# Optimization experiments

Measured on AMD Instinct MI355X. Metric: run time of the kernel, lower is better.

Reference implementation:

```python
import jax, jax.numpy as jnp
import numpy as np

ALPHA = 2.0   # spikingjelly surrogate.ATan default alpha
TAU = 2.0
VTH = 1.0
EPS = 1e-5

@jax.custom_vjp
def atan_spike(x):
    return (x >= 0.0).astype(x.dtype)

def _as_fwd(x):
    return atan_spike(x), x

def _as_bwd(x, g):
    # ATan surrogate derivative: alpha/2 / (1 + (pi/2*alpha*x)^2)
    return (g * (ALPHA / 2.0) / (1.0 + (jnp.pi / 2.0 * ALPHA * x) ** 2),)

atan_spike.defvjp(_as_fwd, _as_bwd)

def lif_multistep(x):
    # x: [B, T, D]; LIF with decay_input=True, v_reset=0 (hard reset), detach_reset=True
    xt = jnp.swapaxes(x, 0, 1)  # [T, B, D] time-major
    def step(v, xi):
        v = v + (xi - v) / TAU                       # integrate with input decay
        s = atan_spike(v - VTH)                       # fire (surrogate grad)
        v = v * (1.0 - jax.lax.stop_gradient(s))      # hard reset to 0, detached
        return v, s
    _, spikes = jax.lax.scan(step, jnp.zeros_like(xt[0]), xt)
    return jnp.swapaxes(spikes, 0, 1)  # [B, T, D]

def layernorm(x, g, b):
    m = x.mean(-1, keepdims=True)
    v = x.var(-1, keepdims=True)
    return (x - m) / jnp.sqrt(v + EPS) * g + b

def setup_inputs() -> dict:
    key = jax.random.key(0)
    ks = jax.random.split(key, 6)
    B, T, IN, HP, E, H, D = 256, 256, 4, 64, 512, 1024, 4
    s = 0.02
    return {
        "hist_feat": jax.random.normal(ks[0], (B, T, IN), jnp.float32),
        "pW1": jax.random.normal(ks[1], (IN, HP), jnp.float32) * s,
        "pb1": jnp.zeros((HP,), jnp.float32),
        "pW2": jax.random.normal(ks[2], (HP, E), jnp.float32) * s,
        "pb2": jnp.zeros((E,), jnp.float32),
        "fc1_w": jax.random.normal(ks[3], (D, E, H), jnp.float32) * s,
        "fc1_b": jnp.zeros((D, H), jnp.float32),
        "ln1_g": jnp.ones((D, H), jnp.float32),
        "ln1_b": jnp.zeros((D, H), jnp.float32),
        "fc2_w": jax.random.normal(ks[4], (D, H, E), jnp.float32) * s,
        "fc2_b": jnp.zeros((D, E), jnp.float32),
        "ln2_g": jnp.ones((D, E), jnp.float32),
        "ln2_b": jnp.zeros((D, E), jnp.float32),
    }

def reference(hist_feat, pW1, pb1, pW2, pb2, fc1_w, fc1_b, ln1_g, ln1_b,
              fc2_w, fc2_b, ln2_g, ln2_b):
    # input projector: Linear -> exact GELU -> Linear
    x = jax.nn.gelu(hist_feat @ pW1 + pb1, approximate=False) @ pW2 + pb2  # [B,T,E]
    depth = fc1_w.shape[0]
    for d in range(depth):  # small fixed layer loop
        res = x
        h = layernorm(x @ fc1_w[d] + fc1_b[d], ln1_g[d], ln1_b[d])  # [B,T,H]
        h = lif_multistep(h)
        h = layernorm(h @ fc2_w[d] + fc2_b[d], ln2_g[d], ln2_b[d])  # [B,T,E]
        h = lif_multistep(h)
        x = res + h  # dropout is identity in eval mode
    return x[:, -1]  # pooling='last', no mask -> last timestep, [B,E]
```

## Files before the change

kernel.cpp:

```cpp
#include <hip/hip_runtime.h>
#include <hip/hip_bf16.h>
#include <math.h>

#define B_  256
#define T_  256
#define IN_ 4
#define HP_ 64
#define E_  512
#define H_  1024
#define D_  4

typedef __hip_bfloat16 bf16;
typedef _Float16 f16;
typedef _Float16 f16x8 __attribute__((ext_vector_type(8)));
typedef float f32x4 __attribute__((ext_vector_type(4)));

__device__ __forceinline__ float load1(const void* p, size_t idx, bool isb) {
    if (isb) {
        unsigned int u = ((const unsigned short*)p)[idx];
        return __uint_as_float(u << 16);
    }
    return ((const float*)p)[idx];
}

__device__ __forceinline__ float4 load4(const void* p, size_t idx, bool isb) {
    if (isb) {
        ushort4 u = *(const ushort4*)((const unsigned short*)p + idx);
        float4 r;
        r.x = __uint_as_float(((unsigned int)u.x) << 16);
        r.y = __uint_as_float(((unsigned int)u.y) << 16);
        r.z = __uint_as_float(((unsigned int)u.z) << 16);
        r.w = __uint_as_float(((unsigned int)u.w) << 16);
        return r;
    }
    return *((const float4*)p + (idx >> 2));
}

__device__ __forceinline__ void split3(float x, f16& h, f16& hs, f16& lb) {
    h = (f16)x;
    float hf = (float)h;
    hs = (f16)(hf * 4.8828125e-4f);
    lb = (f16)((x - hf) * 2048.0f);
}

__global__ void sniff_count_kernel(const unsigned short* __restrict__ p,
                                   int* __restrict__ cnts) {
    __shared__ int cnt;
    if (threadIdx.x == 0) cnt = 0;
    __syncthreads();
    int local = 0;
    #pragma unroll
    for (int k = 0; k < 4; ++k) {
        int i = blockIdx.x * 1024 + k * 256 + threadIdx.x;
        unsigned int bits = ((unsigned int)p[i]) << 16;
        float v = __uint_as_float(bits);
        float a = fabsf(v);
        if (!(a <= 1e4f)) local++;
        else if (v != 0.0f && a < 1e-6f) local++;
    }
    atomicAdd(&cnt, local);
    __syncthreads();
    if (threadIdx.x == 0) cnts[blockIdx.x] = cnt;
}

__global__ void sniff_final_kernel(const int* __restrict__ cnts,
                                   int* __restrict__ flag) {
    int s = 0;
    for (int i = 0; i < 64; ++i) s += cnts[i];
    *flag = (s > 1024) ? 0 : 1;
}

__global__ __launch_bounds__(256) void wsplit_kernel(
        const void* __restrict__ W, size_t wOff, unsigned short* __restrict__ Wt,
        int K, int N, const int* __restrict__ flag) {
    const bool isb = (*flag != 0);
    __shared__ float tile[32][33];
    const int n0 = blockIdx.x * 32, k0 = blockIdx.y * 32;
    const int t = threadIdx.x;
    {
        int lk = t >> 3, ln0 = (t & 7) << 2;
        float4 v = load4(W, wOff + (size_t)(k0 + lk) * N + n0 + ln0, isb);
        tile[lk][ln0 + 0] = v.x; tile[lk][ln0 + 1] = v.y;
        tile[lk][ln0 + 2] = v.z; tile[lk][ln0 + 3] = v.w;
    }
    __syncthreads();
    int n = t >> 3, kq0 = (t & 7) << 2;
    size_t base = (size_t)(n0 + n) * (2 * (size_t)K) + k0 + kq0;
    #pragma unroll
    for (int j = 0; j < 4; ++j) {
        float x = tile[kq0 + j][n];
        f16 h, hs, lb;
        split3(x, h, hs, lb);
        Wt[base + j]     = *(unsigned short*)&h;
        Wt[base + j + K] = *(unsigned short*)&lb;
    }
}

__global__ __launch_bounds__(512, 2) void gemm_mfma3_kernel(
        const unsigned short* __restrict__ At, const unsigned short* __restrict__ Wt,
        const void* __restrict__ bias, size_t bOff,
        float* __restrict__ C, int N, int K, const int* __restrict__ flag) {
    const bool isb = (*flag != 0);
    __shared__ unsigned short As[128 * 64];
    __shared__ unsigned short Bs[128 * 64];

    const int gx = N >> 7;
    const int gy = (int)gridDim.x / gx;
    int bx, by;
    {
        int bid = blockIdx.x;
        if ((gy & 7) == 0) {
            int k = bid & 7, i = bid >> 3;
            bx = i % gx;
            by = (gy >> 3) * k + i / gx;
        } else { bx = bid % gx; by = bid / gx; }
    }
    const int bn = bx * 128;
    const int bm = by * 128;

    const int tid  = threadIdx.x;
    const int lane = tid & 63;
    const int wave = tid >> 6;
    const int wm = wave >> 1;
    const int wn = wave & 1;
    const int g  = lane >> 4;
    const int lr = lane & 15;

    const int sar = tid >> 2;
    const int skq = tid & 3;

    const f16 C11 = (f16)4.8828125e-4f;
    const f16x8 c11v = {C11, C11, C11, C11, C11, C11, C11, C11};

    f32x4 acc[2][4];
    #pragma unroll
    for (int i = 0; i < 2; ++i)
        #pragma unroll
        for (int j = 0; j < 4; ++j) acc[i][j] = (f32x4){0.f, 0.f, 0.f, 0.f};

    const unsigned short* Ap = At + (size_t)(bm + sar) * (2 * (size_t)K) + skq * 8;
    const unsigned short* Wp = Wt + (size_t)(bn + sar) * (2 * (size_t)K) + skq * 8;

    f16x8 av0 = *(const f16x8*)(Ap);
    f16x8 av1 = *(const f16x8*)(Ap + K);
    f16x8 wv0 = *(const f16x8*)(Wp);
    f16x8 wv1 = *(const f16x8*)(Wp + K);

    const int nt = K >> 5;
    for (int t = 0; t < nt; ++t) {
        const int arb = sar * 64, asw = sar & 7;
        *(f16x8*)&As[arb + ((skq ^ asw)) * 8]       = av0;
        *(f16x8*)&As[arb + (((4 | skq) ^ asw)) * 8] = av1;
        *(f16x8*)&Bs[arb + ((skq ^ asw)) * 8]       = wv0;
        *(f16x8*)&Bs[arb + (((4 | skq) ^ asw)) * 8] = wv1;
        __syncthreads();
        if (t + 1 < nt) {
            const int k0 = (t + 1) << 5;
            av0 = *(const f16x8*)(Ap + k0);
            av1 = *(const f16x8*)(Ap + K + k0);
            wv0 = *(const f16x8*)(Wp + k0);
            wv1 = *(const f16x8*)(Wp + K + k0);
        }
        f16x8 a0[2], a2[2], b0[4], b2[4];
        #pragma unroll
        for (int mi = 0; mi < 2; ++mi) {
            const int ar = wm * 32 + mi * 16 + lr;
            a0[mi] = *(const f16x8*)&As[ar * 64 + ((g ^ (ar & 7))) * 8];
            a2[mi] = *(const f16x8*)&As[ar * 64 + (((4 | g) ^ (ar & 7))) * 8];
        }
        #pragma unroll
        for (int ni = 0; ni < 4; ++ni) {
            const int br = wn * 64 + ni * 16 + lr;
            b0[ni] = *(const f16x8*)&Bs[br * 64 + ((g ^ (br & 7))) * 8];
            b2[ni] = *(const f16x8*)&Bs[br * 64 + (((4 | g) ^ (br & 7))) * 8];
        }
        #pragma unroll
        for (int mi = 0; mi < 2; ++mi)
            #pragma unroll
            for (int ni = 0; ni < 4; ++ni)
                acc[mi][ni] = __builtin_amdgcn_mfma_f32_16x16x32_f16(
                    a0[mi], b0[ni], acc[mi][ni], 0, 0, 0);
        {
            f16x8 a1[2];
            #pragma unroll
            for (int mi = 0; mi < 2; ++mi) a1[mi] = a0[mi] * c11v;
            #pragma unroll
            for (int mi = 0; mi < 2; ++mi)
                #pragma unroll
                for (int ni = 0; ni < 4; ++ni)
                    acc[mi][ni] = __builtin_amdgcn_mfma_f32_16x16x32_f16(
                        a1[mi], b2[ni], acc[mi][ni], 0, 0, 0);
        }
        {
            f16x8 b1[4];
            #pragma unroll
            for (int ni = 0; ni < 4; ++ni) b1[ni] = b0[ni] * c11v;
            #pragma unroll
            for (int mi = 0; mi < 2; ++mi)
                #pragma unroll
                for (int ni = 0; ni < 4; ++ni)
                    acc[mi][ni] = __builtin_amdgcn_mfma_f32_16x16x32_f16(
                        a2[mi], b1[ni], acc[mi][ni], 0, 0, 0);
        }
        __syncthreads();
    }
    #pragma unroll
    for (int ni = 0; ni < 4; ++ni) {
        const int col = bn + wn * 64 + ni * 16 + lr;
        const float bv = load1(bias, bOff + col, isb);
        #pragma unroll
        for (int mi = 0; mi < 2; ++mi) {
            #pragma unroll
            for (int r = 0; r < 4; ++r) {
                const size_t row = (size_t)(bm + wm * 32 + mi * 16 + g * 4 + r);
                C[row * N + col] = acc[mi][ni][r] + bv;
            }
        }
    }
}

__global__ __launch_bounds__(256, 3) void gemm_mfma2_kernel(
        const unsigned short* __restrict__ At, const unsigned short* __restrict__ Wt,
        const void* __restrict__ bias, size_t bOff,
        float* __restrict__ C, int N, int K, const int* __restrict__ flag) {
    const bool isb = (*flag != 0);
    __shared__ unsigned short As[2][128 * 64];
    __shared__ unsigned short Bs[2][128 * 64];

    const int gx = N >> 7;
    const int gy = (int)gridDim.x / gx;
    int bx, by;
    {
        int bid = blockIdx.x;
        if ((gy & 7) == 0) {
            int k = bid & 7, i = bid >> 3;
            bx = i % gx;
            by = (gy >> 3) * k + i / gx;
        } else { bx = bid % gx; by = bid / gx; }
    }
    const int bn = bx * 128;
    const int bm = by * 128;

    const int tid  = threadIdx.x;
    const int lane = tid & 63;
    const int wave = tid >> 6;
    const int wm = wave >> 1;
    const int wn = wave & 1;
    const int g  = lane >> 4;
    const int lr = lane & 15;

    const int sar = tid >> 1;
    const int sah = tid & 1;
    const int sbn = tid >> 1;
    const int sq  = tid & 1;

    const f16 C11 = (f16)4.8828125e-4f;
    const f16x8 c11v = {C11, C11, C11, C11, C11, C11, C11, C11};

    f32x4 acc[4][4];
    #pragma unroll
    for (int i = 0; i < 4; ++i)
        #pragma unroll
        for (int j = 0; j < 4; ++j) acc[i][j] = (f32x4){0.f, 0.f, 0.f, 0.f};

    const unsigned short* Ap = At + (size_t)(bm + sar) * (size_t)K + sah * 16;
    const unsigned short* Wp = Wt + (size_t)(bn + sbn) * (2 * (size_t)K) + sq * 16;

    f16x8 av[2], wv[4];
    #pragma unroll
    for (int c = 0; c < 2; ++c)
        av[c] = *(const f16x8*)(Ap + c * 8);
    #pragma unroll
    for (int pl = 0; pl < 2; ++pl)
        #pragma unroll
        for (int c = 0; c < 2; ++c)
            wv[pl * 2 + c] = *(const f16x8*)(Wp + (size_t)pl * K + c * 8);

    const int nt = K >> 5;
    for (int t = 0; t < nt; ++t) {
        const int cur = t & 1;
        const int arb = sar * 64, asw = sar & 7;
        #pragma unroll
        for (int c = 0; c < 2; ++c) {
            const int gg = sah * 2 + c;
            *(f16x8*)&As[cur][arb + ((gg ^ asw)) * 8] = av[c];
        }
        const int brb = sbn * 64, bsw = sbn & 7;
        #pragma unroll
        for (int pl = 0; pl < 2; ++pl)
            #pragma unroll
            for (int c = 0; c < 2; ++c) {
                const int gg = sq * 2 + c;
                *(f16x8*)&Bs[cur][brb + (((pl << 2) | gg) ^ bsw) * 8] = wv[pl * 2 + c];
            }
        __syncthreads();
        if (t + 1 < nt) {
            const int k0 = (t + 1) << 5;
            #pragma unroll
            for (int c = 0; c < 2; ++c)
                av[c] = *(const f16x8*)(Ap + k0 + c * 8);
            #pragma unroll
            for (int pl = 0; pl < 2; ++pl)
                #pragma unroll
                for (int c = 0; c < 2; ++c)
                    wv[pl * 2 + c] = *(const f16x8*)(Wp + (size_t)pl * K + k0 + c * 8);
        }
        f16x8 a0[4], b0[4], b2[4];
        #pragma unroll
        for (int mi = 0; mi < 4; ++mi) {
            const int ar = wm * 64 + mi * 16 + lr;
            a0[mi] = *(const f16x8*)&As[cur][ar * 64 + ((g ^ (ar & 7))) * 8];
        }
        #pragma unroll
        for (int ni = 0; ni < 4; ++ni) {
            const int br = wn * 64 + ni * 16 + lr;
            b0[ni] = *(const f16x8*)&Bs[cur][br * 64 + ((g ^ (br & 7))) * 8];
            b2[ni] = *(const f16x8*)&Bs[cur][br * 64 + (((4 | g) ^ (br & 7))) * 8];
        }
        #pragma unroll
        for (int mi = 0; mi < 4; ++mi)
            #pragma unroll
            for (int ni = 0; ni < 4; ++ni)
                acc[mi][ni] = __builtin_amdgcn_mfma_f32_16x16x32_f16(
                    a0[mi], b0[ni], acc[mi][ni], 0, 0, 0);
        {
            f16x8 a1[4];
            #pragma unroll
            for (int mi = 0; mi < 4; ++mi) a1[mi] = a0[mi] * c11v;
            #pragma unroll
            for (int mi = 0; mi < 4; ++mi)
                #pragma unroll
                for (int ni = 0; ni < 4; ++ni)
                    acc[mi][ni] = __builtin_amdgcn_mfma_f32_16x16x32_f16(
                        a1[mi], b2[ni], acc[mi][ni], 0, 0, 0);
        }
    }
    #pragma unroll
    for (int ni = 0; ni < 4; ++ni) {
        const int col = bn + wn * 64 + ni * 16 + lr;
        const float bv = load1(bias, bOff + col, isb);
        #pragma unroll
        for (int mi = 0; mi < 4; ++mi) {
            #pragma unroll
            for (int r = 0; r < 4; ++r) {
                const size_t row = (size_t)(bm + wm * 64 + mi * 16 + g * 4 + r);
                C[row * N + col] = acc[mi][ni][r] + bv;
            }
        }
    }
}

#define RB_ 16
__global__ __launch_bounds__(256) void proj_kernel(
        const void* __restrict__ hist, const void* __restrict__ pW1,
        const void* __restrict__ pb1,  const void* __restrict__ pW2,
        const void* __restrict__ pb2,  float* __restrict__ Xc,
        unsigned short* __restrict__ At1,
        size_t m0, const int* __restrict__ flag) {
    const bool isb = (*flag != 0);
    __shared__ float h1[RB_][HP_];
    const size_t mb = (size_t)blockIdx.x * RB_;
    const int tid = threadIdx.x;
    const int lane = tid & 63;
    const int grp = tid >> 6;
    #pragma unroll
    for (int rep = 0; rep < 4; ++rep) {
        int idx = tid + rep * 256;
        int r = idx >> 6, c = idx & 63;
        size_t gm = m0 + mb + r;
        float acc = 0.f;
        #pragma unroll
        for (int i = 0; i < IN_; ++i)
            acc = fmaf(load1(hist, gm * IN_ + i, isb),
                       load1(pW1, (size_t)i * HP_ + c, isb), acc);
        acc += load1(pb1, c, isb);
        h1[r][c] = 0.5f * acc * (1.0f + erff(acc * 0.70710678118654752440f));
    }
    __syncthreads();
    const int e0 = lane * 8;
    float acc[4][8];
    #pragma unroll
    for (int r = 0; r < 4; ++r)
        #pragma unroll
        for (int j = 0; j < 8; ++j) acc[r][j] = 0.f;
    for (int i = 0; i < HP_; ++i) {
        float4 wA = load4(pW2, (size_t)i * E_ + e0, isb);
        float4 wB = load4(pW2, (size_t)i * E_ + e0 + 4, isb);
        float w[8] = {wA.x, wA.y, wA.z, wA.w, wB.x, wB.y, wB.z, wB.w};
        #pragma unroll
        for (int r = 0; r < 4; ++r) {
            float h = h1[grp * 4 + r][i];
            #pragma unroll
            for (int j = 0; j < 8; ++j) acc[r][j] = fmaf(h, w[j], acc[r][j]);
        }
    }
    #pragma unroll
    for (int r = 0; r < 4; ++r) {
        size_t row = mb + grp * 4 + r;
        float o[8];
        #pragma unroll
        for (int j = 0; j < 8; ++j)
            o[j] = acc[r][j] + load1(pb2, e0 + j, isb);
        *(float4*)(Xc + row * E_ + e0)     = (float4){o[0], o[1], o[2], o[3]};
        *(float4*)(Xc + row * E_ + e0 + 4) = (float4){o[4], o[5], o[6], o[7]};
        f16x8 hv, lv;
        #pragma unroll
        for (int j = 0; j < 8; ++j) {
            f16 h, hs, lb;
            split3(o[j], h, hs, lb);
            hv[j] = h; lv[j] = lb;
        }
        *(f16x8*)&At1[row * (2 * E_) + e0]      = hv;
        *(f16x8*)&At1[row * (2 * E_) + E_ + e0] = lv;
    }
}

__device__ __forceinline__ float block_sum(float v, float* smem, int tid) {
    #pragma unroll
    for (int off = 32; off > 0; off >>= 1) v += __shfl_down(v, off, 64);
    __syncthreads();
    if ((tid & 63) == 0) smem[tid >> 6] = v;
    __syncthreads();
    if (tid == 0) smem[4] = smem[0] + smem[1] + smem[2] + smem[3];
    __syncthreads();
    return smem[4];
}

__global__ __launch_bounds__(256) void ln_stats_kernel(const float* __restrict__ Y,
                                                       float* __restrict__ stats,
                                                       int N) {
    __shared__ float smem[5];
    size_t row = blockIdx.x;
    const float* y = Y + row * (size_t)N;
    int tid = threadIdx.x;
    int nPer = N >> 8;
    float vals[4];
    float s = 0.f;
    for (int i = 0; i < nPer; ++i) { float v = y[tid + (i << 8)]; vals[i] = v; s += v; }
    float mean = block_sum(s, smem, tid) / (float)N;
    float sq = 0.f;
    for (int i = 0; i < nPer; ++i) { float d0 = vals[i] - mean; sq += d0 * d0; }
    float var = block_sum(sq, smem, tid) / (float)N;
    if (tid == 0) {
        stats[row * 2]     = mean;
        stats[row * 2 + 1] = sqrtf(var + 1e-5f);
    }
}

__global__ __launch_bounds__(64) void lif_kernel(const float* __restrict__ Y,
                                                 const float* __restrict__ stats,
                                                 const void* __restrict__ g, size_t gOff,
                                                 const void* __restrict__ b, size_t bOff,
                                                 unsigned short* __restrict__ At2,
                                                 int N, const int* __restrict__ flag) {
    const bool isb = (*flag != 0);
    int f = blockIdx.x * 64 + threadIdx.x;
    int bb = blockIdx.y;
    const float gw = load1(g, gOff + f, isb);
    const float bw = load1(b, bOff + f, isb);
    size_t base = (size_t)bb * T_ * N + f;
    size_t srow = (size_t)bb * T_;
    float v = 0.f;
    for (int t0 = 0; t0 < T_; t0 += 16) {
        float x[16], mn[16], dn[16], s[16];
        #pragma unroll
        for (int j = 0; j < 16; ++j) {
            x[j]  = Y[base + (size_t)(t0 + j) * N];
            mn[j] = stats[(srow + t0 + j) * 2];
            dn[j] = stats[(srow + t0 + j) * 2 + 1];
        }
        #pragma unroll
        for (int j = 0; j < 16; ++j) {
            float xn = (x[j] - mn[j]) / dn[j] * gw + bw;
            v = v + (xn - v) * 0.5f;
            s[j] = (v - 1.0f >= 0.0f) ? 1.0f : 0.0f;
            v = v * (1.0f - s[j]);
        }
        #pragma unroll
        for (int j = 0; j < 16; ++j) {
            f16 h = (f16)s[j];
            At2[base + (size_t)(t0 + j) * N] = *(unsigned short*)&h;
        }
    }
}

__global__ __launch_bounds__(64) void lif_add_kernel(const float* __restrict__ Z,
                                                     const float* __restrict__ stats,
                                                     const void* __restrict__ g, size_t gOff,
                                                     const void* __restrict__ b, size_t bOff,
                                                     float* __restrict__ Xc,
                                                     unsigned short* __restrict__ At1,
                                                     void* __restrict__ outp, int b0,
                                                     int lastLayer,
                                                     const int* __restrict__ flag) {
    const bool isb = (*flag != 0);
    int e = blockIdx.x * 64 + threadIdx.x;
    int bb = blockIdx.y;
    const float gw = load1(g, gOff + e, isb);
    const float bw = load1(b, bOff + e, isb);
    size_t base  = (size_t)bb * T_ * E_ + e;
    size_t base2 = (size_t)bb * T_ * (2 * E_) + e;
    size_t srow  = (size_t)bb * T_;
    float v = 0.f;
    for (int t0 = 0; t0 < T_; t0 += 16) {
        float x[16], xc[16], mn[16], dn[16], s[16];
        #pragma unroll
        for (int j = 0; j < 16; ++j) {
            x[j]  = Z[base + (size_t)(t0 + j) * E_];
            mn[j] = stats[(srow + t0 + j) * 2];
            dn[j] = stats[(srow + t0 + j) * 2 + 1];
        }
        #pragma unroll
        for (int j = 0; j < 16; ++j) xc[j] = Xc[base + (size_t)(t0 + j) * E_];
        #pragma unroll
        for (int j = 0; j < 16; ++j) {
            float xn = (x[j] - mn[j]) / dn[j] * gw + bw;
            v = v + (xn - v) * 0.5f;
            s[j] = (v - 1.0f >= 0.0f) ? 1.0f : 0.0f;
            v = v * (1.0f - s[j]);
        }
        #pragma unroll
        for (int j = 0; j < 16; ++j) {
            float nx = xc[j] + s[j];
            Xc[base + (size_t)(t0 + j) * E_] = nx;
            f16 h, hs, lb;
            split3(nx, h, hs, lb);
            At1[base2 + (size_t)(t0 + j) * (2 * E_)]      = *(unsigned short*)&h;
            At1[base2 + (size_t)(t0 + j) * (2 * E_) + E_] = *(unsigned short*)&lb;
        }
        if (lastLayer && t0 + 16 == T_) {
            float nx = Xc[base + (size_t)(T_ - 1) * E_];
            size_t oi = (size_t)(b0 + bb) * E_ + e;
            if (isb) ((bf16*)outp)[oi] = __float2bfloat16(nx);
            else     ((float*)outp)[oi] = nx;
        }
    }
}

extern "C" void kernel_launch(void* const* d_in, const int* in_sizes, int n_in,
                              void* d_out, int out_size, void* d_ws, size_t ws_size,
                              hipStream_t stream) {
    char* ws = (char*)d_ws;
    int* flag = (int*)ws;
    int* cnts = (int*)(ws + 64);

    const size_t wtCount = 2 * (size_t)E_ * H_;
    const size_t wtBytes = 2 * D_ * wtCount * sizeof(unsigned short);
    unsigned short* Wt1 = (unsigned short*)(ws + 512);
    unsigned short* Wt2 = Wt1 + (size_t)D_ * wtCount;

    size_t used = 512 + wtBytes;
    size_t avail = (ws_size > used) ? ws_size - used : 0;
    const size_t perBatch = (size_t)T_ * ((E_ + H_ + E_) * 4 + 2 * E_ * 2 + H_ * 2 + 16);
    int CB = 256;
    while (CB > 1 && (size_t)CB * perBatch > avail) CB >>= 1;
    const int R = CB * T_;

    float* Xc  = (float*)(ws + used);
    float* HBc = Xc + (size_t)R * E_;
    float* Y2c = HBc + (size_t)R * H_;
    unsigned short* At1 = (unsigned short*)(Y2c + (size_t)R * E_);
    unsigned short* At2 = At1 + (size_t)R * 2 * E_;
    float* St1 = (float*)(At2 + (size_t)R * H_);
    float* St2 = St1 + (size_t)R * 2;

    sniff_count_kernel<<<64, 256, 0, stream>>>((const unsigned short*)d_in[0], cnts);
    sniff_final_kernel<<<1, 1, 0, stream>>>(cnts, flag);

    for (int d = 0; d < D_; ++d) {
        wsplit_kernel<<<dim3(H_ / 32, E_ / 32), 256, 0, stream>>>(
            d_in[5], (size_t)d * E_ * H_, Wt1 + (size_t)d * wtCount, E_, H_, flag);
        wsplit_kernel<<<dim3(E_ / 32, H_ / 32), 256, 0, stream>>>(
            d_in[9], (size_t)d * H_ * E_, Wt2 + (size_t)d * wtCount, H_, E_, flag);
    }

    for (int b0 = 0; b0 < B_; b0 += CB) {
        proj_kernel<<<R / RB_, 256, 0, stream>>>(d_in[0], d_in[1], d_in[2], d_in[3],
                                                 d_in[4], Xc, At1, (size_t)b0 * T_, flag);
        for (int d = 0; d < D_; ++d) {
            size_t b1o = (size_t)d * H_;
            size_t b2o = (size_t)d * E_;

            gemm_mfma3_kernel<<<(H_ / 128) * (R / 128), 512, 0, stream>>>(
                At1, Wt1 + (size_t)d * wtCount, d_in[6], b1o, HBc, H_, E_, flag);
            ln_stats_kernel<<<R, 256, 0, stream>>>(HBc, St1, H_);
            lif_kernel<<<dim3(H_ / 64, CB), 64, 0, stream>>>(
                HBc, St1, d_in[7], b1o, d_in[8], b1o, At2, H_, flag);

            gemm_mfma2_kernel<<<(E_ / 128) * (R / 128), 256, 0, stream>>>(
                At2, Wt2 + (size_t)d * wtCount, d_in[10], b2o, Y2c, E_, H_, flag);
            ln_stats_kernel<<<R, 256, 0, stream>>>(Y2c, St2, E_);
            lif_add_kernel<<<dim3(E_ / 64, CB), 64, 0, stream>>>(
                Y2c, St2, d_in[11], b2o, d_in[12], b2o, Xc, At1,
                d_out, b0, (d == D_ - 1) ? 1 : 0, flag);
        }
    }
}
```

Measured before the change: 3.437 ms.

## Fuse layernorm partial sums into GEMM epilogues and replace stats pass

The GEMM epilogues now compute per-row partial sums and sums of squares over each wave's 64 columns, reduce them with lane shuffles, and write them to a small partial buffer. A tiny finalize kernel then combines the partials into mean and rstd, replacing the separate layernorm-stats kernels that re-read the full HBc and Y2c activations. This removes a full read of the GEMM outputs per layer. In exchange, variance now comes from the single-pass E[x^2]-mean^2 formula, which is less numerically stable, and the epilogues do extra shuffles.

```diff
diff --git a/kernel.cpp b/kernel.cpp
--- a/kernel.cpp
+++ b/kernel.cpp
@@ -96,10 +96,27 @@
     }
 }
 
+__global__ __launch_bounds__(256) void ln_fin_kernel(const float* __restrict__ P,
+                                                     int ns, float* __restrict__ stats,
+                                                     int N) {
+    int row = blockIdx.x * 256 + threadIdx.x;
+    const float* p = P + (size_t)row * ns * 2;
+    float s = 0.f, s2 = 0.f;
+    for (int i = 0; i < ns; ++i) {
+        s  += p[i * 2];
+        s2 += p[i * 2 + 1];
+    }
+    float mean = s / (float)N;
+    float var  = fmaxf(s2 / (float)N - mean * mean, 0.f);
+    stats[row * 2]     = mean;
+    stats[row * 2 + 1] = sqrtf(var + 1e-5f);
+}
+
 __global__ __launch_bounds__(512, 2) void gemm_mfma3_kernel(
         const unsigned short* __restrict__ At, const unsigned short* __restrict__ Wt,
         const void* __restrict__ bias, size_t bOff,
-        float* __restrict__ C, int N, int K, const int* __restrict__ flag) {
+        float* __restrict__ C, float* __restrict__ Pt,
+        int N, int K, const int* __restrict__ flag) {
     const bool isb = (*flag != 0);
     __shared__ unsigned short As[128 * 64];
     __shared__ unsigned short Bs[128 * 64];
@@ -204,16 +221,33 @@
         }
         __syncthreads();
     }
-    #pragma unroll
-    for (int ni = 0; ni < 4; ++ni) {
-        const int col = bn + wn * 64 + ni * 16 + lr;
-        const float bv = load1(bias, bOff + col, isb);
-        #pragma unroll
-        for (int mi = 0; mi < 2; ++mi) {
-            #pragma unroll
-            for (int r = 0; r < 4; ++r) {
-                const size_t row = (size_t)(bm + wm * 32 + mi * 16 + g * 4 + r);
-                C[row * N + col] = acc[mi][ni][r] + bv;
+    const int nslot = gx * 2;
+    float bvv[4];
+    #pragma unroll
+    for (int ni = 0; ni < 4; ++ni)
+        bvv[ni] = load1(bias, bOff + bn + wn * 64 + ni * 16 + lr, isb);
+    #pragma unroll
+    for (int mi = 0; mi < 2; ++mi) {
+        #pragma unroll
+        for (int r = 0; r < 4; ++r) {
+            const size_t row = (size_t)(bm + wm * 32 + mi * 16 + g * 4 + r);
+            float s = 0.f, s2 = 0.f;
+            #pragma unroll
+            for (int ni = 0; ni < 4; ++ni) {
+                const int col = bn + wn * 64 + ni * 16 + lr;
+                float o = acc[mi][ni][r] + bvv[ni];
+                C[row * N + col] = o;
+                s += o; s2 = fmaf(o, o, s2);
+            }
+            #pragma unroll
+            for (int off = 1; off < 16; off <<= 1) {
+                s  += __shfl_xor(s,  off, 64);
+                s2 += __shfl_xor(s2, off, 64);
+            }
+            if (lr == 0) {
+                const int slot = bx * 2 + wn;
+                Pt[row * (size_t)(2 * nslot) + slot * 2]     = s;
+                Pt[row * (size_t)(2 * nslot) + slot * 2 + 1] = s2;
             }
         }
     }
@@ -222,7 +256,8 @@
 __global__ __launch_bounds__(256, 3) void gemm_mfma2_kernel(
         const unsigned short* __restrict__ At, const unsigned short* __restrict__ Wt,
         const void* __restrict__ bias, size_t bOff,
-        float* __restrict__ C, int N, int K, const int* __restrict__ flag) {
+        float* __restrict__ C, float* __restrict__ Pt,
+        int N, int K, const int* __restrict__ flag) {
     const bool isb = (*flag != 0);
     __shared__ unsigned short As[2][128 * 64];
     __shared__ unsigned short Bs[2][128 * 64];
@@ -335,16 +370,33 @@
                         a1[mi], b2[ni], acc[mi][ni], 0, 0, 0);
         }
     }
-    #pragma unroll
-    for (int ni = 0; ni < 4; ++ni) {
-        const int col = bn + wn * 64 + ni * 16 + lr;
-        const float bv = load1(bias, bOff + col, isb);
-        #pragma unroll
-        for (int mi = 0; mi < 4; ++mi) {
-            #pragma unroll
-            for (int r = 0; r < 4; ++r) {
-                const size_t row = (size_t)(bm + wm * 64 + mi * 16 + g * 4 + r);
-                C[row * N + col] = acc[mi][ni][r] + bv;
+    const int nslot = gx * 2;
+    float bvv[4];
+    #pragma unroll
+    for (int ni = 0; ni < 4; ++ni)
+        bvv[ni] = load1(bias, bOff + bn + wn * 64 + ni * 16 + lr, isb);
+    #pragma unroll
+    for (int mi = 0; mi < 4; ++mi) {
+        #pragma unroll
+        for (int r = 0; r < 4; ++r) {
+            const size_t row = (size_t)(bm + wm * 64 + mi * 16 + g * 4 + r);
+            float s = 0.f, s2 = 0.f;
+            #pragma unroll
+            for (int ni = 0; ni < 4; ++ni) {
+                const int col = bn + wn * 64 + ni * 16 + lr;
+                float o = acc[mi][ni][r] + bvv[ni];
+                C[row * N + col] = o;
+                s += o; s2 = fmaf(o, o, s2);
+            }
+            #pragma unroll
+            for (int off = 1; off < 16; off <<= 1) {
+                s  += __shfl_xor(s,  off, 64);
+                s2 += __shfl_xor(s2, off, 64);
+            }
+            if (lr == 0) {
+                const int slot = bx * 2 + wn;
+                Pt[row * (size_t)(2 * nslot) + slot * 2]     = s;
+                Pt[row * (size_t)(2 * nslot) + slot * 2 + 1] = s2;
             }
         }
     }
@@ -412,38 +464,6 @@
         }
         *(f16x8*)&At1[row * (2 * E_) + e0]      = hv;
         *(f16x8*)&At1[row * (2 * E_) + E_ + e0] = lv;
-    }
-}
-
-__device__ __forceinline__ float block_sum(float v, float* smem, int tid) {
-    #pragma unroll
-    for (int off = 32; off > 0; off >>= 1) v += __shfl_down(v, off, 64);
-    __syncthreads();
-    if ((tid & 63) == 0) smem[tid >> 6] = v;
-    __syncthreads();
-    if (tid == 0) smem[4] = smem[0] + smem[1] + smem[2] + smem[3];
-    __syncthreads();
-    return smem[4];
-}
-
-__global__ __launch_bounds__(256) void ln_stats_kernel(const float* __restrict__ Y,
-                                                       float* __restrict__ stats,
-                                                       int N) {
-    __shared__ float smem[5];
-    size_t row = blockIdx.x;
-    const float* y = Y + row * (size_t)N;
-    int tid = threadIdx.x;
-    int nPer = N >> 8;
-    float vals[4];
-    float s = 0.f;
-    for (int i = 0; i < nPer; ++i) { float v = y[tid + (i << 8)]; vals[i] = v; s += v; }
-    float mean = block_sum(s, smem, tid) / (float)N;
-    float sq = 0.f;
-    for (int i = 0; i < nPer; ++i) { float d0 = vals[i] - mean; sq += d0 * d0; }
-    float var = block_sum(sq, smem, tid) / (float)N;
-    if (tid == 0) {
-        stats[row * 2]     = mean;
-        stats[row * 2 + 1] = sqrtf(var + 1e-5f);
     }
 }
 
@@ -551,7 +571,8 @@
 
     size_t used = 512 + wtBytes;
     size_t avail = (ws_size > used) ? ws_size - used : 0;
-    const size_t perBatch = (size_t)T_ * ((E_ + H_ + E_) * 4 + 2 * E_ * 2 + H_ * 2 + 16);
+    const size_t perBatch = (size_t)T_ * ((E_ + H_ + E_) * 4 + 2 * E_ * 2 + H_ * 2
+                                          + 16 + (32 + 16) * 4);
     int CB = 256;
     while (CB > 1 && (size_t)CB * perBatch > avail) CB >>= 1;
     const int R = CB * T_;
@@ -563,6 +584,8 @@
     unsigned short* At2 = At1 + (size_t)R * 2 * E_;
     float* St1 = (float*)(At2 + (size_t)R * H_);
     float* St2 = St1 + (size_t)R * 2;
+    float* Pt1 = St2 + (size_t)R * 2;
+    float* Pt2 = Pt1 + (size_t)R * 32;
 
     sniff_count_kernel<<<64, 256, 0, stream>>>((const unsigned short*)d_in[0], cnts);
     sniff_final_kernel<<<1, 1, 0, stream>>>(cnts, flag);
@@ -582,14 +605,14 @@
             size_t b2o = (size_t)d * E_;
 
             gemm_mfma3_kernel<<<(H_ / 128) * (R / 128), 512, 0, stream>>>(
-                At1, Wt1 + (size_t)d * wtCount, d_in[6], b1o, HBc, H_, E_, flag);
-            ln_stats_kernel<<<R, 256, 0, stream>>>(HBc, St1, H_);
+                At1, Wt1 + (size_t)d * wtCount, d_in[6], b1o, HBc, Pt1, H_, E_, flag);
+            ln_fin_kernel<<<R / 256, 256, 0, stream>>>(Pt1, 16, St1, H_);
             lif_kernel<<<dim3(H_ / 64, CB), 64, 0, stream>>>(
                 HBc, St1, d_in[7], b1o, d_in[8], b1o, At2, H_, flag);
 
             gemm_mfma2_kernel<<<(E_ / 128) * (R / 128), 256, 0, stream>>>(
-                At2, Wt2 + (size_t)d * wtCount, d_in[10], b2o, Y2c, E_, H_, flag);
-            ln_stats_kernel<<<R, 256, 0, stream>>>(Y2c, St2, E_);
+                At2, Wt2 + (size_t)d * wtCount, d_in[10], b2o, Y2c, Pt2, E_, H_, flag);
+            ln_fin_kernel<<<R / 256, 256, 0, stream>>>(Pt2, 8, St2, E_);
             lif_add_kernel<<<dim3(E_ / 64, CB), 64, 0, stream>>>(
                 Y2c, St2, d_in[11], b2o, d_in[12], b2o, Xc, At1,
                 d_out, b0, (d == D_ - 1) ? 1 : 0, flag);
```

After: 2.951 ms. 1.16x faster.
